# Optimization experiments

Measured on AMD Instinct MI355X. Metric: run time of the kernel, lower is better.

Reference implementation:

```python
import jax, jax.numpy as jnp
import numpy as np

B, C, H, W = 16, 256, 224, 224

def border_mask(h, w, dtype=jnp.float32):
    # Bresenham lines along the 4 edges of the rectangle == 1-pixel border ring.
    ys = jnp.arange(h)
    xs = jnp.arange(w)
    on_border = (ys[:, None] == 0) | (ys[:, None] == h - 1) | (xs[None, :] == 0) | (xs[None, :] == w - 1)
    return on_border.astype(dtype)  # [H, W]

def setup_inputs() -> dict:
    key = jax.random.key(0)
    k1, k2 = jax.random.split(key)
    x = jax.random.normal(k1, (B, C, H, W), dtype=jnp.float32)
    conv_w = jax.random.normal(k2, (1, C, 1, 1), dtype=jnp.float32) * (1.0 / np.sqrt(C))
    conv_b = jnp.zeros((1,), dtype=jnp.float32)
    return {"x": x, "conv_w": conv_w, "conv_b": conv_b}

def reference(x, conv_w, conv_b):
    # 1x1 conv to a single channel: contraction over C.
    w = conv_w[0, :, 0, 0]  # [C]
    att = jnp.einsum('bchw,c->bhw', x, w) + conv_b[0]  # [B,H,W]
    att = jax.nn.sigmoid(att)
    mask = border_mask(x.shape[2], x.shape[3], x.dtype)  # [H,W], identical for all batches
    combined = att * (1.0 + mask)  # [B,H,W]
    return x * combined[:, None, :, :]  # [B,C,H,W]
```

## Files before the change

kernel.cpp:

```cpp
#include <hip/hip_runtime.h>

constexpr int C  = 256;
constexpr int H  = 224;
constexpr int W  = 224;
constexpr int HW = H * W;
constexpr int PIX = 64;
constexpr int THREADS = 256;
constexpr int TILES_PER_B = HW / PIX;
constexpr int BATCH = 16;

typedef float f32x4 __attribute__((ext_vector_type(4)));

__global__ __launch_bounds__(THREADS, 4)
void fused_sigmoid_border_scale(const float* __restrict__ x,
                                const float* __restrict__ wv,
                                const float* __restrict__ bv,
                                float* __restrict__ out)
{
    __shared__ f32x4 pw[4][16];
    __shared__ float comb[PIX];

    const int t   = threadIdx.x;
    const int blk = blockIdx.x;
    const int b   = blk / TILES_PER_B;
    const int hw0 = (blk - b * TILES_PER_B) * PIX;

    const float* xb = x   + (size_t)b * C * HW + hw0;
    float*       ob = out + (size_t)b * C * HW + hw0;

    const int q    = t & 15;
    const int c0   = t >> 4;
    const int wave = t >> 6;

    f32x4 v[16];
    #pragma unroll
    for (int k = 0; k < 16; ++k) {
        const int c = k * 16 + c0;
        v[k] = __builtin_nontemporal_load(
            reinterpret_cast<const f32x4*>(xb + (size_t)c * HW + q * 4));
    }

    f32x4 acc = (f32x4)(0.f);
    #pragma unroll
    for (int k = 0; k < 16; ++k) {
        const float wk = wv[k * 16 + c0];
        acc.x = fmaf(v[k].x, wk, acc.x);
        acc.y = fmaf(v[k].y, wk, acc.y);
        acc.z = fmaf(v[k].z, wk, acc.z);
        acc.w = fmaf(v[k].w, wk, acc.w);
    }

    #pragma unroll
    for (int m = 16; m <= 32; m <<= 1) {
        acc.x += __shfl_xor(acc.x, m);
        acc.y += __shfl_xor(acc.y, m);
        acc.z += __shfl_xor(acc.z, m);
        acc.w += __shfl_xor(acc.w, m);
    }
    if ((t & 63) < 16) pw[wave][q] = acc;
    __syncthreads();

    if (t < PIX) {
        const int qq = t >> 2, cc = t & 3;
        float s = pw[0][qq][cc] + pw[1][qq][cc] + pw[2][qq][cc] + pw[3][qq][cc]
                + bv[0];
        const float att = 1.0f / (1.0f + expf(-s));
        const int hw = hw0 + t;
        const int h  = hw / W;
        const int w  = hw - h * W;
        const bool border = (h == 0) | (h == H - 1) | (w == 0) | (w == W - 1);
        comb[t] = att * (border ? 2.0f : 1.0f);
    }
    __syncthreads();

    const f32x4 m4 = *reinterpret_cast<const f32x4*>(&comb[q * 4]);
    #pragma unroll
    for (int k = 0; k < 16; ++k) {
        const int c = k * 16 + c0;
        f32x4 r = v[k] * m4;
        __builtin_nontemporal_store(r,
            reinterpret_cast<f32x4*>(ob + (size_t)c * HW + q * 4));
    }
}

extern "C" void kernel_launch(void* const* d_in, const int* in_sizes, int n_in,
                              void* d_out, int out_size, void* d_ws, size_t ws_size,
                              hipStream_t stream) {
    const float* x  = (const float*)d_in[0];
    const float* wv = (const float*)d_in[1];
    const float* bv = (const float*)d_in[2];
    float* out = (float*)d_out;

    dim3 grid(BATCH * TILES_PER_B);
    fused_sigmoid_border_scale<<<grid, THREADS, 0, stream>>>(x, wv, bv, out);
}
```

Before: 314.6 us.

## Wave-local channel reduction with persistent grid-stride tiles, removing LDS and barriers

Each wave now owns 16 pixels and reduces across channels entirely with cross-lane shuffles, so each lane computes the sigmoid and border mask for its own four pixels. This removes the shared-memory staging and both block barriers. The kernel also becomes persistent: a fixed grid of 1024 blocks loops over tiles with the conv weights held in registers, which avoids reloading them per tile. The trade-off is that each row load now covers only 64 contiguous bytes per channel instead of 256, and a small fixed grid may leave less memory parallelism in flight.

Result: slower. 578.7 us (+83.9%).

```diff
diff --git a/kernel.cpp b/kernel.cpp
--- a/kernel.cpp
+++ b/kernel.cpp
@@ -8,6 +8,8 @@
 constexpr int THREADS = 256;
 constexpr int TILES_PER_B = HW / PIX;
 constexpr int BATCH = 16;
+constexpr int TILES = BATCH * TILES_PER_B;
+constexpr int GRID = 1024;
 
 typedef float f32x4 __attribute__((ext_vector_type(4)));
 
@@ -17,69 +19,69 @@
                                 const float* __restrict__ bv,
                                 float* __restrict__ out)
 {
-    __shared__ f32x4 pw[4][16];
-    __shared__ float comb[PIX];
+    const int t    = threadIdx.x;
+    const int wave = t >> 6;
+    const int lane = t & 63;
+    const int q    = lane & 3;
+    const int cg   = lane >> 2;
 
-    const int t   = threadIdx.x;
-    const int blk = blockIdx.x;
-    const int b   = blk / TILES_PER_B;
-    const int hw0 = (blk - b * TILES_PER_B) * PIX;
+    const float b0 = bv[0];
 
-    const float* xb = x   + (size_t)b * C * HW + hw0;
-    float*       ob = out + (size_t)b * C * HW + hw0;
+    float wk[16];
+    #pragma unroll
+    for (int k = 0; k < 16; ++k) wk[k] = wv[k * 16 + cg];
 
-    const int q    = t & 15;
-    const int c0   = t >> 4;
-    const int wave = t >> 6;
+    for (int tile = blockIdx.x; tile < TILES; tile += GRID) {
+        const int b   = tile / TILES_PER_B;
+        const int hw0 = (tile - b * TILES_PER_B) * PIX;
+        const int px  = hw0 + wave * 16 + q * 4;
 
-    f32x4 v[16];
-    #pragma unroll
-    for (int k = 0; k < 16; ++k) {
-        const int c = k * 16 + c0;
-        v[k] = __builtin_nontemporal_load(
-            reinterpret_cast<const f32x4*>(xb + (size_t)c * HW + q * 4));
-    }
+        const float* xb = x   + (size_t)b * C * HW + px;
+        float*       ob = out + (size_t)b * C * HW + px;
 
-    f32x4 acc = (f32x4)(0.f);
-    #pragma unroll
-    for (int k = 0; k < 16; ++k) {
-        const float wk = wv[k * 16 + c0];
-        acc.x = fmaf(v[k].x, wk, acc.x);
-        acc.y = fmaf(v[k].y, wk, acc.y);
-        acc.z = fmaf(v[k].z, wk, acc.z);
-        acc.w = fmaf(v[k].w, wk, acc.w);
-    }
+        f32x4 v[16];
+        #pragma unroll
+        for (int k = 0; k < 16; ++k) {
+            const int c = k * 16 + cg;
+            v[k] = __builtin_nontemporal_load(
+                reinterpret_cast<const f32x4*>(xb + (size_t)c * HW));
+        }
 
-    #pragma unroll
-    for (int m = 16; m <= 32; m <<= 1) {
-        acc.x += __shfl_xor(acc.x, m);
-        acc.y += __shfl_xor(acc.y, m);
-        acc.z += __shfl_xor(acc.z, m);
-        acc.w += __shfl_xor(acc.w, m);
-    }
-    if ((t & 63) < 16) pw[wave][q] = acc;
-    __syncthreads();
+        f32x4 acc = (f32x4)(0.f);
+        #pragma unroll
+        for (int k = 0; k < 16; ++k) {
+            acc.x = fmaf(v[k].x, wk[k], acc.x);
+            acc.y = fmaf(v[k].y, wk[k], acc.y);
+            acc.z = fmaf(v[k].z, wk[k], acc.z);
+            acc.w = fmaf(v[k].w, wk[k], acc.w);
+        }
 
-    if (t < PIX) {
-        const int qq = t >> 2, cc = t & 3;
-        float s = pw[0][qq][cc] + pw[1][qq][cc] + pw[2][qq][cc] + pw[3][qq][cc]
-                + bv[0];
-        const float att = 1.0f / (1.0f + expf(-s));
-        const int hw = hw0 + t;
-        const int h  = hw / W;
-        const int w  = hw - h * W;
-        const bool border = (h == 0) | (h == H - 1) | (w == 0) | (w == W - 1);
-        comb[t] = att * (border ? 2.0f : 1.0f);
-    }
-    __syncthreads();
+        #pragma unroll
+        for (int m = 4; m <= 32; m <<= 1) {
+            acc.x += __shfl_xor(acc.x, m);
+            acc.y += __shfl_xor(acc.y, m);
+            acc.z += __shfl_xor(acc.z, m);
+            acc.w += __shfl_xor(acc.w, m);
+        }
 
-    const f32x4 m4 = *reinterpret_cast<const f32x4*>(&comb[q * 4]);
-    #pragma unroll
-    for (int k = 0; k < 16; ++k) {
-        const int c = k * 16 + c0;
-        f32x4 r = v[k] * m4;
-        __builtin_nontemporal_store(r,
-            reinterpret_cast<f32x4*>(ob + (size_t)c * HW + q * 4));
+        f32x4 comb;
+        #pragma unroll
+        for (int j = 0; j < 4; ++j) {
+            const float s   = acc[j] + b0;
+            const float att = 1.0f / (1.0f + expf(-s));
+            const int hw = px + j;
+            const int h  = hw / W;
+            const int w  = hw - h * W;
+            const bool border = (h == 0) | (h == H - 1) | (w == 0) | (w == W - 1);
+            comb[j] = att * (border ? 2.0f : 1.0f);
+        }
+
+        #pragma unroll
+        for (int k = 0; k < 16; ++k) {
+            const int c = k * 16 + cg;
+            __builtin_nontemporal_store(v[k] * comb,
+                reinterpret_cast<f32x4*>(ob + (size_t)c * HW));
+        }
     }
 }
 
@@ -91,6 +93,5 @@
     const float* bv = (const float*)d_in[2];
     float* out = (float*)d_out;
 
-    dim3 grid(BATCH * TILES_PER_B);
-    fused_sigmoid_border_scale<<<grid, THREADS, 0, stream>>>(x, wv, bv, out);
+    fused_sigmoid_border_scale<<<dim3(GRID), dim3(THREADS), 0, stream>>>(x, wv, bv, out);
 }
```
